# Kernel optimization log

Measured on AMD Instinct MI355X. Metric: run time of the kernel, lower is better.

The kernel has to match this reference:

```python
import jax, jax.numpy as jnp
import numpy as np

D = 1024   # dim_embedding
H = 16     # n_head
HD = D // H


def setup_inputs() -> dict:
    key = jax.random.key(0)
    ks = jax.random.split(key, 5)
    B, T = 2, 2048
    x = jax.random.normal(ks[0], (B, T, D), dtype=jnp.float32)
    e = jax.random.normal(ks[1], (B, T, D), dtype=jnp.float32)
    s = 0.02
    W_en = jax.random.normal(ks[2], (D, 2 * D), dtype=jnp.float32) * s   # c_attn_en (k,v from encoder)
    W_q = jax.random.normal(ks[3], (D, D), dtype=jnp.float32) * s        # c_attn (q from decoder)
    W_o = jax.random.normal(ks[4], (D, D), dtype=jnp.float32) * s        # c_proj
    return {"x": x, "e": e, "W_en": W_en, "W_q": W_q, "W_o": W_o}


def reference(x, e, W_en, W_q, W_o):
    B, T, C = e.shape
    kv = e @ W_en                       # [B,T,2C]
    k, v = jnp.split(kv, 2, axis=-1)    # [B,T,C] each
    q = x @ W_q                         # [B,T,C]
    # reshape to heads: [B,H,T,hd]
    q = q.reshape(B, T, H, HD).transpose(0, 2, 1, 3)
    k = k.reshape(B, T, H, HD).transpose(0, 2, 1, 3)
    v = v.reshape(B, T, H, HD).transpose(0, 2, 1, 3)
    att = jnp.einsum("bhqd,bhkd->bhqk", q, k) * (1.0 / jnp.sqrt(jnp.float32(HD)))
    att = jax.nn.softmax(att, axis=-1)  # dropout=0 (eval)
    y = jnp.einsum("bhqk,bhkd->bhqd", att, v)
    y = y.transpose(0, 2, 1, 3).reshape(B, T, C)
    return y @ W_o
```

## Files before the change

### kernel.cpp

```cpp
#include <hip/hip_runtime.h>

typedef unsigned short u16;
typedef unsigned int u32;
typedef __bf16 bf16x8 __attribute__((ext_vector_type(8)));
typedef float f32x4 __attribute__((ext_vector_type(4)));
typedef float f32x16 __attribute__((ext_vector_type(16)));

#define D_EMB 1024
#define T_SEQ 2048
#define NH 16
#define HD 64

#define GLB(p) ((const __attribute__((address_space(1))) unsigned int*)(p))
#define LDSP(p) ((__attribute__((address_space(3))) unsigned int*)(p))
#define VMCNT(n) asm volatile("s_waitcnt vmcnt(" #n ")" ::: "memory")
#define LGKM0() asm volatile("s_waitcnt lgkmcnt(0)" ::: "memory")

__device__ __forceinline__ u16 f2bf(float f) {
  union { float f; unsigned u; } c; c.f = f;
  unsigned u = c.u;
  unsigned r = (u + 0x7FFFu + ((u >> 16) & 1u)) >> 16;
  return (u16)r;
}
__device__ __forceinline__ u32 fbits(float f) {
  union { float f; unsigned u; } c; c.f = f; return c.u;
}

__global__ __launch_bounds__(256) void prep_kernel(
    const float* __restrict__ x, const float* __restrict__ e,
    const float* __restrict__ W_q, const float* __restrict__ W_en, const float* __restrict__ W_o,
    u16* __restrict__ xb, u16* __restrict__ eb,
    u16* __restrict__ Wqt, u16* __restrict__ Went, u16* __restrict__ Wot) {
  __shared__ float tile[32][33];
  const int bid = blockIdx.x, tid = threadIdx.x;
  if (bid < 8192) {
    const float* in = (bid < 4096) ? x : e;
    u16* out = (bid < 4096) ? xb : eb;
    int i = (bid & 4095) * 256 + tid;
    float4 v = reinterpret_cast<const float4*>(in)[i];
    ushort4 o;
    o.x = f2bf(v.x); o.y = f2bf(v.y); o.z = f2bf(v.z); o.w = f2bf(v.w);
    reinterpret_cast<ushort4*>(out)[i] = o;
    return;
  }
  const float* in; u16* out; int K, N, bx, by;
  int rem = bid - 8192;
  if (rem < 1024)      { in = W_q;  out = Wqt;  K = 1024; N = 1024; bx = rem & 31; by = rem >> 5; }
  else if (rem < 3072) { int r2 = rem - 1024; in = W_en; out = Went; K = 1024; N = 2048; bx = r2 & 63; by = r2 >> 6; }
  else                 { int r3 = rem - 3072; in = W_o;  out = Wot;  K = 1024; N = 1024; bx = r3 & 31; by = r3 >> 5; }
  int tx = tid & 31, ty = tid >> 5;
  int n0 = bx * 32, k0 = by * 32;
#pragma unroll
  for (int s = 0; s < 4; s++)
    tile[ty + 8 * s][tx] = in[(size_t)(k0 + ty + 8 * s) * N + n0 + tx];
  __syncthreads();
#pragma unroll
  for (int s = 0; s < 4; s++)
    out[(size_t)(n0 + ty + 8 * s) * K + k0 + tx] = f2bf(tile[tx][ty + 8 * s]);
}

__global__ __launch_bounds__(256) void proj_kernel(
    const u16* __restrict__ xb, const u16* __restrict__ eb,
    const u16* __restrict__ Wqt, const u16* __restrict__ Went,
    u16* __restrict__ qw, u16* __restrict__ kw, u16* __restrict__ vTw) {
  __shared__ u16 Al[3][128 * 32], Bl[3][128 * 32];
  const int tid = threadIdx.x;
  const int nb = blockIdx.x, mb = blockIdx.y;
  const int wave = tid >> 6, lane = tid & 63;
  const int ln15 = lane & 15, quad = lane >> 4;
  const int wm = wave & 1, wn = wave >> 1;

  const u16* A = (nb < 8) ? xb : eb;
  const u16* Wt = (nb < 8) ? (Wqt + (size_t)nb * 128 * D_EMB)
                           : (Went + ((size_t)nb * 128 - D_EMB) * D_EMB);

  const int srow = lane >> 2, sch = lane & 3;
  const int gch = sch ^ ((srow >> 1) & 3);
  const u16* gA = A + (size_t)(mb * 128 + wave * 32 + srow) * D_EMB + gch * 8;
  const u16* gB = Wt + (size_t)(wave * 32 + srow) * D_EMB + gch * 8;

  auto stage = [&](int kb, u16* AL, u16* BL) {
    char* lA = (char*)AL + wave * 2048;
    char* lB = (char*)BL + wave * 2048;
#pragma unroll
    for (int it = 0; it < 2; it++) {
      __builtin_amdgcn_global_load_lds(GLB(gA + (size_t)it * 16 * D_EMB + kb), LDSP(lA + it * 1024), 16, 0, 0);
      __builtin_amdgcn_global_load_lds(GLB(gB + (size_t)it * 16 * D_EMB + kb), LDSP(lB + it * 1024), 16, 0, 0);
    }
  };

  f32x4 acc[4][4] = {};
  bf16x8 af[4], bfr[4];

  auto ldfrag = [&](const u16* AL, const u16* BL) {
#pragma unroll
    for (int mt = 0; mt < 4; mt++) {
      int r = wm * 64 + mt * 16 + ln15;
      af[mt] = *reinterpret_cast<const bf16x8*>(&AL[r * 32 + ((quad ^ ((r >> 1) & 3)) * 8)]);
    }
#pragma unroll
    for (int nt = 0; nt < 4; nt++) {
      int r = wn * 64 + nt * 16 + ln15;
      bfr[nt] = *reinterpret_cast<const bf16x8*>(&BL[r * 32 + ((quad ^ ((r >> 1) & 3)) * 8)]);
    }
  };
  auto domfma = [&]() {
    __builtin_amdgcn_s_setprio(1);
#pragma unroll
    for (int mt = 0; mt < 4; mt++)
#pragma unroll
      for (int nt = 0; nt < 4; nt++)
        acc[mt][nt] = __builtin_amdgcn_mfma_f32_16x16x32_bf16(af[mt], bfr[nt], acc[mt][nt], 0, 0, 0);
    __builtin_amdgcn_s_setprio(0);
  };

  stage(0,  Al[0], Bl[0]);
  stage(32, Al[1], Bl[1]);
  stage(64, Al[2], Bl[2]);
  u16 *cA = Al[0], *cB = Bl[0], *nA = Al[1], *nB = Bl[1], *mA = Al[2], *mB = Bl[2];

  for (int kb = 0; kb < 928; kb += 32) {
    VMCNT(8);
    __builtin_amdgcn_s_barrier();
    ldfrag(cA, cB);
    LGKM0();
    __builtin_amdgcn_s_barrier();
    stage(kb + 96, cA, cB);
    domfma();
    u16* t;
    t = cA; cA = nA; nA = mA; mA = t;
    t = cB; cB = nB; nB = mB; mB = t;
  }
  VMCNT(8); __builtin_amdgcn_s_barrier(); ldfrag(cA, cB); domfma();
  VMCNT(4); __builtin_amdgcn_s_barrier(); ldfrag(nA, nB); domfma();
  VMCNT(0); __builtin_amdgcn_s_barrier(); ldfrag(mA, mB); domfma();

  const float QSCL = 0.125f * 1.44269504f;
#pragma unroll
  for (int mt = 0; mt < 4; mt++) {
#pragma unroll
    for (int nt = 0; nt < 4; nt++) {
#pragma unroll
      for (int i = 0; i < 4; i++) {
        int rr = mb * 128 + wm * 64 + mt * 16 + quad * 4 + i;
        int c  = nb * 128 + wn * 64 + nt * 16 + ln15;
        float v = acc[mt][nt][i];
        int b = rr >> 11, t = rr & 2047;
        if (c < D_EMB) {
          int h = c >> 6, d = c & 63;
          qw[(((size_t)(b * NH + h)) * T_SEQ + t) * HD + d] = f2bf(v * QSCL);
        } else if (c < 2 * D_EMB) {
          int cc = c - D_EMB; int h = cc >> 6, d = cc & 63;
          kw[(((size_t)(b * NH + h)) * T_SEQ + t) * HD + d] = f2bf(v);
        } else {
          int cc = c - 2 * D_EMB; int h = cc >> 6, d = cc & 63;
          vTw[(((size_t)(b * NH + h)) * HD + d) * T_SEQ + t] = f2bf(v);
        }
      }
    }
  }
}

__global__ __launch_bounds__(256) void attn_kernel(
    const u16* __restrict__ q, const u16* __restrict__ k,
    const u16* __restrict__ vT, u16* __restrict__ y) {
  __shared__ u16 Kl[3][64][64], Vl[3][64][64];

  const int bh = blockIdx.y;
  const int qt = blockIdx.x;
  const int tid = threadIdx.x;
  const int wave = tid >> 6, lane = tid & 63;
  const int q32 = lane & 31, hi = lane >> 5;
  const int b = bh >> 4, h = bh & 15;

  const int pq = (q32 & 19) | ((q32 & 8) >> 1) | ((q32 & 4) << 1);
  const int pq7 = pq & 7;

  const int qrow = qt * 128 + wave * 32 + q32;
  const u16* qbase = q + ((size_t)bh * T_SEQ + qrow) * HD;
  bf16x8 qf[4];
#pragma unroll
  for (int s = 0; s < 4; s++)
    qf[s] = *reinterpret_cast<const bf16x8*>(qbase + s * 16 + hi * 8);

  f32x16 o2[2] = {};
  float lp = 0.f;

  const int srow = (lane >> 3) & 7;
  const int gch  = (lane & 7) ^ srow;
  const u16* kg0 = k  + ((size_t)bh * T_SEQ + wave * 16 + srow) * HD + gch * 8;
  const u16* vg0 = vT + ((size_t)bh * HD + wave * 16 + srow) * T_SEQ + gch * 8;

  auto issue_dma = [&](int t, u16 (*KL)[64], u16 (*VL)[64]) {
    char* klb = (char*)KL + wave * 2048;
    char* vlb = (char*)VL + wave * 2048;
    const u16* kp = kg0 + (size_t)t * 64 * HD;
    const u16* vp = vg0 + t * 64;
    __builtin_amdgcn_global_load_lds(GLB(kp),             LDSP(klb),        16, 0, 0);
    __builtin_amdgcn_global_load_lds(GLB(kp + 8 * HD),    LDSP(klb + 1024), 16, 0, 0);
    __builtin_amdgcn_global_load_lds(GLB(vp),             LDSP(vlb),        16, 0, 0);
    __builtin_amdgcn_global_load_lds(GLB(vp + 8 * T_SEQ), LDSP(vlb + 1024), 16, 0, 0);
  };

  auto body = [&](const u16 (*KL)[64], const u16 (*VL)[64]) {
    f32x16 s2[2] = {};
#pragma unroll
    for (int s = 0; s < 4; s++)
#pragma unroll
      for (int kt2 = 0; kt2 < 2; kt2++) {
        int r = kt2 * 32 + pq;
        bf16x8 kf = *reinterpret_cast<const bf16x8*>(&KL[r][(((s * 2 + hi) ^ pq7) * 8)]);
        s2[kt2] = __builtin_amdgcn_mfma_f32_32x32x16_bf16(kf, qf[s], s2[kt2], 0, 0, 0);
      }

#pragma unroll
    for (int s = 0; s < 4; s++) {
      const int kt2 = s >> 1;
      const int g0 = (2 * s) & 3;
      float e0 = __builtin_amdgcn_exp2f(s2[kt2][4 * g0 + 0]);
      float e1 = __builtin_amdgcn_exp2f(s2[kt2][4 * g0 + 1]);
      float e2 = __builtin_amdgcn_exp2f(s2[kt2][4 * g0 + 2]);
      float e3 = __builtin_amdgcn_exp2f(s2[kt2][4 * g0 + 3]);
      float e4 = __builtin_amdgcn_exp2f(s2[kt2][4 * g0 + 4]);
      float e5 = __builtin_amdgcn_exp2f(s2[kt2][4 * g0 + 5]);
      float e6 = __builtin_amdgcn_exp2f(s2[kt2][4 * g0 + 6]);
      float e7 = __builtin_amdgcn_exp2f(s2[kt2][4 * g0 + 7]);
      lp += ((e0 + e1) + (e2 + e3)) + ((e4 + e5) + (e6 + e7));
      u32 w0 = __builtin_amdgcn_perm(fbits(e1), fbits(e0), 0x07060302u);
      u32 w1 = __builtin_amdgcn_perm(fbits(e3), fbits(e2), 0x07060302u);
      u32 w2 = __builtin_amdgcn_perm(fbits(e5), fbits(e4), 0x07060302u);
      u32 w3 = __builtin_amdgcn_perm(fbits(e7), fbits(e6), 0x07060302u);
      union { u32 w[4]; bf16x8 v; } pu;
      pu.w[0] = w0; pu.w[1] = w1; pu.w[2] = w2; pu.w[3] = w3;
      bf16x8 pf = pu.v;
#pragma unroll
      for (int dt = 0; dt < 2; dt++) {
        int r = dt * 32 + q32;
        bf16x8 vf = *reinterpret_cast<const bf16x8*>(&VL[r][(((s * 2 + hi) ^ (r & 7)) * 8)]);
        o2[dt] = __builtin_amdgcn_mfma_f32_32x32x16_bf16(vf, pf, o2[dt], 0, 0, 0);
      }
    }
  };

  issue_dma(0, Kl[0], Vl[0]);
  issue_dma(1, Kl[1], Vl[1]);
  issue_dma(2, Kl[2], Vl[2]);
  u16 (*cK)[64] = Kl[0]; u16 (*cV)[64] = Vl[0];
  u16 (*nK)[64] = Kl[1]; u16 (*nV)[64] = Vl[1];
  u16 (*mK)[64] = Kl[2]; u16 (*mV)[64] = Vl[2];

  for (int t = 0; t < 29; t++) {
    VMCNT(8);
    __builtin_amdgcn_s_barrier();
    body(cK, cV);
    LGKM0();
    __builtin_amdgcn_s_barrier();
    issue_dma(t + 3, cK, cV);
    u16 (*tp)[64];
    tp = cK; cK = nK; nK = mK; mK = tp;
    tp = cV; cV = nV; nV = mV; mV = tp;
  }
  VMCNT(8); __builtin_amdgcn_s_barrier(); body(cK, cV);
  VMCNT(4); __builtin_amdgcn_s_barrier(); body(nK, nV);
  VMCNT(0); __builtin_amdgcn_s_barrier(); body(mK, mV);

  lp += __shfl_xor(lp, 32, 64);
  const float inv = 1.0f / lp;

  const size_t ybase = ((size_t)b * T_SEQ + qrow) * D_EMB + h * 64;
#pragma unroll
  for (int dt = 0; dt < 2; dt++)
#pragma unroll
    for (int g = 0; g < 4; g++) {
      u16 b0 = f2bf(o2[dt][4 * g + 0] * inv), b1 = f2bf(o2[dt][4 * g + 1] * inv);
      u16 b2 = f2bf(o2[dt][4 * g + 2] * inv), b3 = f2bf(o2[dt][4 * g + 3] * inv);
      u32 dw0 = (u32)b0 | ((u32)b1 << 16);
      u32 dw1 = (u32)b2 | ((u32)b3 << 16);
      *reinterpret_cast<uint2*>(&y[ybase + dt * 32 + 8 * g + 4 * hi]) = make_uint2(dw0, dw1);
    }
}

__global__ __launch_bounds__(256) void oproj_kernel(
    const u16* __restrict__ yw, const u16* __restrict__ Wot, float* __restrict__ out) {
  __shared__ u16 Al[3][64 * 32], Bl[3][128 * 32];
  const int tid = threadIdx.x;
  const int nb = blockIdx.x, mb = blockIdx.y;
  const int wave = tid >> 6, lane = tid & 63;
  const int ln15 = lane & 15, quad = lane >> 4;
  const int wm = wave & 1, wn = wave >> 1;

  const int srow = lane >> 2, sch = lane & 3;
  const int gch = sch ^ ((srow >> 1) & 3);
  const u16* gA = yw  + (size_t)(mb * 64 + wave * 16 + srow) * D_EMB + gch * 8;
  const u16* gB = Wot + (size_t)(nb * 128 + wave * 32 + srow) * D_EMB + gch * 8;

  auto stage = [&](int kb, u16* AL, u16* BL) {
    char* lA = (char*)AL + wave * 1024;
    char* lB = (char*)BL + wave * 2048;
    __builtin_amdgcn_global_load_lds(GLB(gA + kb), LDSP(lA), 16, 0, 0);
#pragma unroll
    for (int it = 0; it < 2; it++)
      __builtin_amdgcn_global_load_lds(GLB(gB + (size_t)it * 16 * D_EMB + kb), LDSP(lB + it * 1024), 16, 0, 0);
  };

  f32x4 acc[2][4] = {};
  bf16x8 af[2], bfr[4];

  auto ldfrag = [&](const u16* AL, const u16* BL) {
#pragma unroll
    for (int mt = 0; mt < 2; mt++) {
      int r = wm * 32 + mt * 16 + ln15;
      af[mt] = *reinterpret_cast<const bf16x8*>(&AL[r * 32 + ((quad ^ ((r >> 1) & 3)) * 8)]);
    }
#pragma unroll
    for (int nt = 0; nt < 4; nt++) {
      int r = wn * 64 + nt * 16 + ln15;
      bfr[nt] = *reinterpret_cast<const bf16x8*>(&BL[r * 32 + ((quad ^ ((r >> 1) & 3)) * 8)]);
    }
  };
  auto domfma = [&]() {
    __builtin_amdgcn_s_setprio(1);
#pragma unroll
    for (int mt = 0; mt < 2; mt++)
#pragma unroll
      for (int nt = 0; nt < 4; nt++)
        acc[mt][nt] = __builtin_amdgcn_mfma_f32_16x16x32_bf16(af[mt], bfr[nt], acc[mt][nt], 0, 0, 0);
    __builtin_amdgcn_s_setprio(0);
  };

  stage(0,  Al[0], Bl[0]);
  stage(32, Al[1], Bl[1]);
  stage(64, Al[2], Bl[2]);
  u16 *cA = Al[0], *cB = Bl[0], *nA = Al[1], *nB = Bl[1], *mA = Al[2], *mB = Bl[2];

  for (int kb = 0; kb < 928; kb += 32) {
    VMCNT(6);
    __builtin_amdgcn_s_barrier();
    ldfrag(cA, cB);
    LGKM0();
    __builtin_amdgcn_s_barrier();
    stage(kb + 96, cA, cB);
    domfma();
    u16* t;
    t = cA; cA = nA; nA = mA; mA = t;
    t = cB; cB = nB; nB = mB; mB = t;
  }
  VMCNT(6); __builtin_amdgcn_s_barrier(); ldfrag(cA, cB); domfma();
  VMCNT(3); __builtin_amdgcn_s_barrier(); ldfrag(nA, nB); domfma();
  VMCNT(0); __builtin_amdgcn_s_barrier(); ldfrag(mA, mB); domfma();

#pragma unroll
  for (int mt = 0; mt < 2; mt++)
#pragma unroll
    for (int nt = 0; nt < 4; nt++)
#pragma unroll
      for (int i = 0; i < 4; i++) {
        int rr = mb * 64 + wm * 32 + mt * 16 + quad * 4 + i;
        int c  = nb * 128 + wn * 64 + nt * 16 + ln15;
        out[(size_t)rr * D_EMB + c] = acc[mt][nt][i];
      }
}

extern "C" void kernel_launch(void* const* d_in, const int* in_sizes, int n_in,
                              void* d_out, int out_size, void* d_ws, size_t ws_size,
                              hipStream_t stream) {
  const float* x    = (const float*)d_in[0];
  const float* e    = (const float*)d_in[1];
  const float* W_en = (const float*)d_in[2];
  const float* W_q  = (const float*)d_in[3];
  const float* W_o  = (const float*)d_in[4];
  float* out = (float*)d_out;

  char* w = (char*)d_ws;
  u16* xb   = (u16*)(w);
  u16* eb   = (u16*)(w + (8u  << 20));
  u16* Wqt  = (u16*)(w + (16u << 20));
  u16* Went = (u16*)(w + (18u << 20));
  u16* Wot  = (u16*)(w + (22u << 20));
  u16* qw   = (u16*)(w + (24u << 20));
  u16* kw   = (u16*)(w + (32u << 20));
  u16* vT   = (u16*)(w + (40u << 20));
  u16* yw   = (u16*)(w + (48u << 20));

  prep_kernel<<<12288, 256, 0, stream>>>(x, e, W_q, W_en, W_o, xb, eb, Wqt, Went, Wot);
  proj_kernel<<<dim3(24, 32), 256, 0, stream>>>(xb, eb, Wqt, Went, qw, kw, vT);
  attn_kernel<<<dim3(T_SEQ / 128, 32), 256, 0, stream>>>(qw, kw, vT, yw);
  oproj_kernel<<<dim3(8, 64), 256, 0, stream>>>(yw, Wot, out);
}
```

Baseline: 195.9 us.

## Split attention KV across wave pairs, remap blocks per XCD, shrink projection tiles

The attention kernel now handles 64 query rows per block, with two wave pairs each processing alternating 32-key tiles. Their partial outputs and row sums are combined through LDS at the end. The grid is flattened to 1024 blocks and mapped so each XCD works on contiguous heads for better L2 locality. The projection GEMM moves to 64-row M tiles with double buffering instead of triple, doubling the block count to raise occupancy. In exchange it adds an LDS reduction step and shallower prefetch.

```diff
diff --git a/kernel.cpp b/kernel.cpp
--- a/kernel.cpp
+++ b/kernel.cpp
@@ -63,7 +63,7 @@
     const u16* __restrict__ xb, const u16* __restrict__ eb,
     const u16* __restrict__ Wqt, const u16* __restrict__ Went,
     u16* __restrict__ qw, u16* __restrict__ kw, u16* __restrict__ vTw) {
-  __shared__ u16 Al[3][128 * 32], Bl[3][128 * 32];
+  __shared__ u16 Al[2][64 * 32], Bl[2][128 * 32];
   const int tid = threadIdx.x;
   const int nb = blockIdx.x, mb = blockIdx.y;
   const int wave = tid >> 6, lane = tid & 63;
@@ -76,26 +76,25 @@
 
   const int srow = lane >> 2, sch = lane & 3;
   const int gch = sch ^ ((srow >> 1) & 3);
-  const u16* gA = A + (size_t)(mb * 128 + wave * 32 + srow) * D_EMB + gch * 8;
+  const u16* gA = A + (size_t)(mb * 64 + wave * 16 + srow) * D_EMB + gch * 8;
   const u16* gB = Wt + (size_t)(wave * 32 + srow) * D_EMB + gch * 8;
 
   auto stage = [&](int kb, u16* AL, u16* BL) {
-    char* lA = (char*)AL + wave * 2048;
+    char* lA = (char*)AL + wave * 1024;
     char* lB = (char*)BL + wave * 2048;
-#pragma unroll
-    for (int it = 0; it < 2; it++) {
-      __builtin_amdgcn_global_load_lds(GLB(gA + (size_t)it * 16 * D_EMB + kb), LDSP(lA + it * 1024), 16, 0, 0);
+    __builtin_amdgcn_global_load_lds(GLB(gA + kb), LDSP(lA), 16, 0, 0);
+#pragma unroll
+    for (int it = 0; it < 2; it++)
       __builtin_amdgcn_global_load_lds(GLB(gB + (size_t)it * 16 * D_EMB + kb), LDSP(lB + it * 1024), 16, 0, 0);
-    }
-  };
-
-  f32x4 acc[4][4] = {};
-  bf16x8 af[4], bfr[4];
+  };
+
+  f32x4 acc[2][4] = {};
+  bf16x8 af[2], bfr[4];
 
   auto ldfrag = [&](const u16* AL, const u16* BL) {
 #pragma unroll
-    for (int mt = 0; mt < 4; mt++) {
-      int r = wm * 64 + mt * 16 + ln15;
+    for (int mt = 0; mt < 2; mt++) {
+      int r = wm * 32 + mt * 16 + ln15;
       af[mt] = *reinterpret_cast<const bf16x8*>(&AL[r * 32 + ((quad ^ ((r >> 1) & 3)) * 8)]);
     }
 #pragma unroll
@@ -107,7 +106,7 @@
   auto domfma = [&]() {
     __builtin_amdgcn_s_setprio(1);
 #pragma unroll
-    for (int mt = 0; mt < 4; mt++)
+    for (int mt = 0; mt < 2; mt++)
 #pragma unroll
       for (int nt = 0; nt < 4; nt++)
         acc[mt][nt] = __builtin_amdgcn_mfma_f32_16x16x32_bf16(af[mt], bfr[nt], acc[mt][nt], 0, 0, 0);
@@ -116,33 +115,27 @@
 
   stage(0,  Al[0], Bl[0]);
   stage(32, Al[1], Bl[1]);
-  stage(64, Al[2], Bl[2]);
-  u16 *cA = Al[0], *cB = Bl[0], *nA = Al[1], *nB = Bl[1], *mA = Al[2], *mB = Bl[2];
-
-  for (int kb = 0; kb < 928; kb += 32) {
-    VMCNT(8);
-    __builtin_amdgcn_s_barrier();
-    ldfrag(cA, cB);
+  for (int p = 0; p < 30; p++) {
+    u16* AL = Al[p & 1]; u16* BL = Bl[p & 1];
+    VMCNT(3);
+    __builtin_amdgcn_s_barrier();
+    ldfrag(AL, BL);
     LGKM0();
     __builtin_amdgcn_s_barrier();
-    stage(kb + 96, cA, cB);
+    stage(32 * (p + 2), AL, BL);
     domfma();
-    u16* t;
-    t = cA; cA = nA; nA = mA; mA = t;
-    t = cB; cB = nB; nB = mB; mB = t;
-  }
-  VMCNT(8); __builtin_amdgcn_s_barrier(); ldfrag(cA, cB); domfma();
-  VMCNT(4); __builtin_amdgcn_s_barrier(); ldfrag(nA, nB); domfma();
-  VMCNT(0); __builtin_amdgcn_s_barrier(); ldfrag(mA, mB); domfma();
+  }
+  VMCNT(3); __builtin_amdgcn_s_barrier(); ldfrag(Al[0], Bl[0]); domfma();
+  VMCNT(0); __builtin_amdgcn_s_barrier(); ldfrag(Al[1], Bl[1]); domfma();
 
   const float QSCL = 0.125f * 1.44269504f;
 #pragma unroll
-  for (int mt = 0; mt < 4; mt++) {
+  for (int mt = 0; mt < 2; mt++) {
 #pragma unroll
     for (int nt = 0; nt < 4; nt++) {
 #pragma unroll
       for (int i = 0; i < 4; i++) {
-        int rr = mb * 128 + wm * 64 + mt * 16 + quad * 4 + i;
+        int rr = mb * 64 + wm * 32 + mt * 16 + quad * 4 + i;
         int c  = nb * 128 + wn * 64 + nt * 16 + ln15;
         float v = acc[mt][nt][i];
         int b = rr >> 11, t = rr & 2047;
@@ -164,19 +157,24 @@
 __global__ __launch_bounds__(256) void attn_kernel(
     const u16* __restrict__ q, const u16* __restrict__ k,
     const u16* __restrict__ vT, u16* __restrict__ y) {
-  __shared__ u16 Kl[3][64][64], Vl[3][64][64];
-
-  const int bh = blockIdx.y;
-  const int qt = blockIdx.x;
+  __shared__ u16 Kl[2][2][32 * 64];
+  __shared__ u16 Vl[2][2][64 * 32];
+
+  const int bid = blockIdx.x;
+  const int xcd = bid & 7, jj = bid >> 3;
+  const int bh = xcd * 4 + (jj >> 5);
+  const int qt = jj & 31;
   const int tid = threadIdx.x;
   const int wave = tid >> 6, lane = tid & 63;
   const int q32 = lane & 31, hi = lane >> 5;
+  const int qhalf = wave & 1, pr = wave >> 1;
   const int b = bh >> 4, h = bh & 15;
 
   const int pq = (q32 & 19) | ((q32 & 8) >> 1) | ((q32 & 4) << 1);
   const int pq7 = pq & 7;
-
-  const int qrow = qt * 128 + wave * 32 + q32;
+  const int vsw = (q32 >> 1) & 3;
+
+  const int qrow = qt * 64 + qhalf * 32 + q32;
   const u16* qbase = q + ((size_t)bh * T_SEQ + qrow) * HD;
   bf16x8 qf[4];
 #pragma unroll
@@ -186,45 +184,47 @@
   f32x16 o2[2] = {};
   float lp = 0.f;
 
-  const int srow = (lane >> 3) & 7;
-  const int gch  = (lane & 7) ^ srow;
-  const u16* kg0 = k  + ((size_t)bh * T_SEQ + wave * 16 + srow) * HD + gch * 8;
-  const u16* vg0 = vT + ((size_t)bh * HD + wave * 16 + srow) * T_SEQ + gch * 8;
-
-  auto issue_dma = [&](int t, u16 (*KL)[64], u16 (*VL)[64]) {
-    char* klb = (char*)KL + wave * 2048;
-    char* vlb = (char*)VL + wave * 2048;
-    const u16* kp = kg0 + (size_t)t * 64 * HD;
-    const u16* vp = vg0 + t * 64;
-    __builtin_amdgcn_global_load_lds(GLB(kp),             LDSP(klb),        16, 0, 0);
-    __builtin_amdgcn_global_load_lds(GLB(kp + 8 * HD),    LDSP(klb + 1024), 16, 0, 0);
-    __builtin_amdgcn_global_load_lds(GLB(vp),             LDSP(vlb),        16, 0, 0);
-    __builtin_amdgcn_global_load_lds(GLB(vp + 8 * T_SEQ), LDSP(vlb + 1024), 16, 0, 0);
-  };
-
-  auto body = [&](const u16 (*KL)[64], const u16 (*VL)[64]) {
-    f32x16 s2[2] = {};
-#pragma unroll
-    for (int s = 0; s < 4; s++)
-#pragma unroll
-      for (int kt2 = 0; kt2 < 2; kt2++) {
-        int r = kt2 * 32 + pq;
-        bf16x8 kf = *reinterpret_cast<const bf16x8*>(&KL[r][(((s * 2 + hi) ^ pq7) * 8)]);
-        s2[kt2] = __builtin_amdgcn_mfma_f32_32x32x16_bf16(kf, qf[s], s2[kt2], 0, 0, 0);
-      }
-
+  const u16* khead = k + (size_t)bh * T_SEQ * HD;
+  const u16* vhead = vT + (size_t)bh * HD * T_SEQ;
+  const int kr = lane >> 3;
+  const int kc = (lane & 7) ^ kr;
+  const u16* kg0 = khead + (size_t)(qhalf * 16 + kr) * HD + kc * 8;
+  const int vr = lane >> 2;
+  const int vc = (lane & 3) ^ ((lane >> 3) & 3);
+  const u16* vg0 = vhead + (size_t)(qhalf * 32 + vr) * T_SEQ + vc * 8;
+
+  auto stage = [&](int tile, int buf) {
+    char* kb = (char*)&Kl[pr][buf][0] + qhalf * 2048;
+    char* vb = (char*)&Vl[pr][buf][0] + qhalf * 2048;
+    const u16* kp = kg0 + (size_t)tile * 32 * HD;
+    const u16* vp = vg0 + tile * 32;
+    __builtin_amdgcn_global_load_lds(GLB(kp),              LDSP(kb),        16, 0, 0);
+    __builtin_amdgcn_global_load_lds(GLB(kp + 8 * HD),     LDSP(kb + 1024), 16, 0, 0);
+    __builtin_amdgcn_global_load_lds(GLB(vp),              LDSP(vb),        16, 0, 0);
+    __builtin_amdgcn_global_load_lds(GLB(vp + 16 * T_SEQ), LDSP(vb + 1024), 16, 0, 0);
+  };
+
+  auto body = [&](int buf) {
+    const u16* KL = &Kl[pr][buf][0];
+    const u16* VL = &Vl[pr][buf][0];
+    f32x16 s2 = {};
+    __builtin_amdgcn_s_setprio(1);
 #pragma unroll
     for (int s = 0; s < 4; s++) {
-      const int kt2 = s >> 1;
-      const int g0 = (2 * s) & 3;
-      float e0 = __builtin_amdgcn_exp2f(s2[kt2][4 * g0 + 0]);
-      float e1 = __builtin_amdgcn_exp2f(s2[kt2][4 * g0 + 1]);
-      float e2 = __builtin_amdgcn_exp2f(s2[kt2][4 * g0 + 2]);
-      float e3 = __builtin_amdgcn_exp2f(s2[kt2][4 * g0 + 3]);
-      float e4 = __builtin_amdgcn_exp2f(s2[kt2][4 * g0 + 4]);
-      float e5 = __builtin_amdgcn_exp2f(s2[kt2][4 * g0 + 5]);
-      float e6 = __builtin_amdgcn_exp2f(s2[kt2][4 * g0 + 6]);
-      float e7 = __builtin_amdgcn_exp2f(s2[kt2][4 * g0 + 7]);
+      bf16x8 kf = *reinterpret_cast<const bf16x8*>(&KL[pq * 64 + (((2 * s + hi) ^ pq7) * 8)]);
+      s2 = __builtin_amdgcn_mfma_f32_32x32x16_bf16(kf, qf[s], s2, 0, 0, 0);
+    }
+#pragma unroll
+    for (int sp = 0; sp < 2; sp++) {
+      const int g0 = 2 * sp;
+      float e0 = __builtin_amdgcn_exp2f(s2[4 * g0 + 0]);
+      float e1 = __builtin_amdgcn_exp2f(s2[4 * g0 + 1]);
+      float e2 = __builtin_amdgcn_exp2f(s2[4 * g0 + 2]);
+      float e3 = __builtin_amdgcn_exp2f(s2[4 * g0 + 3]);
+      float e4 = __builtin_amdgcn_exp2f(s2[4 * g0 + 4]);
+      float e5 = __builtin_amdgcn_exp2f(s2[4 * g0 + 5]);
+      float e6 = __builtin_amdgcn_exp2f(s2[4 * g0 + 6]);
+      float e7 = __builtin_amdgcn_exp2f(s2[4 * g0 + 7]);
       lp += ((e0 + e1) + (e2 + e3)) + ((e4 + e5) + (e6 + e7));
       u32 w0 = __builtin_amdgcn_perm(fbits(e1), fbits(e0), 0x07060302u);
       u32 w1 = __builtin_amdgcn_perm(fbits(e3), fbits(e2), 0x07060302u);
@@ -236,48 +236,53 @@
 #pragma unroll
       for (int dt = 0; dt < 2; dt++) {
         int r = dt * 32 + q32;
-        bf16x8 vf = *reinterpret_cast<const bf16x8*>(&VL[r][(((s * 2 + hi) ^ (r & 7)) * 8)]);
+        bf16x8 vf = *reinterpret_cast<const bf16x8*>(&VL[r * 32 + (((2 * sp + hi) ^ vsw) * 8)]);
         o2[dt] = __builtin_amdgcn_mfma_f32_32x32x16_bf16(vf, pf, o2[dt], 0, 0, 0);
       }
     }
-  };
-
-  issue_dma(0, Kl[0], Vl[0]);
-  issue_dma(1, Kl[1], Vl[1]);
-  issue_dma(2, Kl[2], Vl[2]);
-  u16 (*cK)[64] = Kl[0]; u16 (*cV)[64] = Vl[0];
-  u16 (*nK)[64] = Kl[1]; u16 (*nV)[64] = Vl[1];
-  u16 (*mK)[64] = Kl[2]; u16 (*mV)[64] = Vl[2];
-
-  for (int t = 0; t < 29; t++) {
-    VMCNT(8);
-    __builtin_amdgcn_s_barrier();
-    body(cK, cV);
+    __builtin_amdgcn_s_setprio(0);
+  };
+
+  stage(pr, 0);
+  stage(2 + pr, 1);
+  for (int ph = 0; ph < 30; ph++) {
+    VMCNT(4);
+    __builtin_amdgcn_s_barrier();
+    body(ph & 1);
     LGKM0();
     __builtin_amdgcn_s_barrier();
-    issue_dma(t + 3, cK, cV);
-    u16 (*tp)[64];
-    tp = cK; cK = nK; nK = mK; mK = tp;
-    tp = cV; cV = nV; nV = mV; mV = tp;
-  }
-  VMCNT(8); __builtin_amdgcn_s_barrier(); body(cK, cV);
-  VMCNT(4); __builtin_amdgcn_s_barrier(); body(nK, nV);
-  VMCNT(0); __builtin_amdgcn_s_barrier(); body(mK, mV);
+    stage(2 * (ph + 2) + pr, ph & 1);
+  }
+  VMCNT(4); __builtin_amdgcn_s_barrier(); body(0);
+  VMCNT(0); __builtin_amdgcn_s_barrier(); body(1);
 
   lp += __shfl_xor(lp, 32, 64);
-  const float inv = 1.0f / lp;
-
-  const size_t ybase = ((size_t)b * T_SEQ + qrow) * D_EMB + h * 64;
-#pragma unroll
-  for (int dt = 0; dt < 2; dt++)
-#pragma unroll
-    for (int g = 0; g < 4; g++) {
-      u16 b0 = f2bf(o2[dt][4 * g + 0] * inv), b1 = f2bf(o2[dt][4 * g + 1] * inv);
-      u16 b2 = f2bf(o2[dt][4 * g + 2] * inv), b3 = f2bf(o2[dt][4 * g + 3] * inv);
-      u32 dw0 = (u32)b0 | ((u32)b1 << 16);
-      u32 dw1 = (u32)b2 | ((u32)b3 << 16);
-      *reinterpret_cast<uint2*>(&y[ybase + dt * 32 + 8 * g + 4 * hi]) = make_uint2(dw0, dw1);
-    }
+  __syncthreads();
+  float* mo = (float*)&Kl[0][0][0];
+  float* ml = (float*)&Vl[0][0][0];
+  if (pr == 1) {
+    f32x16* dst = (f32x16*)(mo + qhalf * 2048 + lane * 32);
+    dst[0] = o2[0]; dst[1] = o2[1];
+    ml[qhalf * 64 + lane] = lp;
+  }
+  __syncthreads();
+  if (pr == 0) {
+    const f32x16* src = (const f32x16*)(mo + qhalf * 2048 + lane * 32);
+    o2[0] += src[0]; o2[1] += src[1];
+    lp += ml[qhalf * 64 + lane];
+    const float inv = 1.0f / lp;
+    const size_t ybase = ((size_t)b * T_SEQ + qrow) * D_EMB + h * 64;
+#pragma unroll
+    for (int dt = 0; dt < 2; dt++)
+#pragma unroll
+      for (int g = 0; g < 4; g++) {
+        u16 b0 = f2bf(o2[dt][4 * g + 0] * inv), b1 = f2bf(o2[dt][4 * g + 1] * inv);
+        u16 b2 = f2bf(o2[dt][4 * g + 2] * inv), b3 = f2bf(o2[dt][4 * g + 3] * inv);
+        u32 dw0 = (u32)b0 | ((u32)b1 << 16);
+        u32 dw1 = (u32)b2 | ((u32)b3 << 16);
+        *reinterpret_cast<uint2*>(&y[ybase + dt * 32 + 8 * g + 4 * hi]) = make_uint2(dw0, dw1);
+      }
+  }
 }
 
 __global__ __launch_bounds__(256) void oproj_kernel(
@@ -383,7 +388,7 @@
   u16* yw   = (u16*)(w + (48u << 20));
 
   prep_kernel<<<12288, 256, 0, stream>>>(x, e, W_q, W_en, W_o, xb, eb, Wqt, Went, Wot);
-  proj_kernel<<<dim3(24, 32), 256, 0, stream>>>(xb, eb, Wqt, Went, qw, kw, vT);
-  attn_kernel<<<dim3(T_SEQ / 128, 32), 256, 0, stream>>>(qw, kw, vT, yw);
+  proj_kernel<<<dim3(24, 64), 256, 0, stream>>>(xb, eb, Wqt, Went, qw, kw, vT);
+  attn_kernel<<<1024, 256, 0, stream>>>(qw, kw, vT, yw);
   oproj_kernel<<<dim3(8, 64), 256, 0, stream>>>(yw, Wot, out);
 }
```

After: 216.3 us. 1.1x slower.
